# Performance work log

Hardware: AMD Instinct MI355X
Metric: run time of the kernel (lower is better)

## Reference

```python
import jax, jax.numpy as jnp
import numpy as np

B, S, I = 64, 32, 64
N_ITEMS = 100000
E, H = 256, 128


def setup_inputs() -> dict:
    key = jax.random.key(0)
    k_len, k_ids, k_ut, k_emb, k_wih, k_whh, k_a1, k_a2, k_vt = jax.random.split(key, 9)
    n_sess = B * S
    # ragged session lengths in [2, I] -> trailing zero padding, all sessions valid
    lengths = jax.random.randint(k_len, (n_sess,), 2, I + 1)
    ids = jax.random.randint(k_ids, (n_sess, I), 1, N_ITEMS + 1)
    pad_mask = jnp.arange(I)[None, :] < lengths[:, None]
    item_id = (ids * pad_mask).reshape(B, S, I).astype(jnp.int32)
    eval_from = jnp.zeros((B,), dtype=jnp.int32)
    u_type = jax.random.randint(k_ut, (B,), 0, 5).astype(jnp.int32)
    sc = 0.05
    emb = jax.random.normal(k_emb, (N_ITEMS + 1, E), jnp.float32) * sc
    emb = emb.at[0].set(0.0)  # padding_idx=0
    W_ih = jax.random.normal(k_wih, (3 * H, E), jnp.float32) * sc
    W_hh = jax.random.normal(k_whh, (3 * H, H), jnp.float32) * sc
    b_ih = jnp.zeros((3 * H,), jnp.float32)
    b_hh = jnp.zeros((3 * H,), jnp.float32)
    W_a1 = jax.random.normal(k_a1, (H, H), jnp.float32) * sc
    W_a2 = jax.random.normal(k_a2, (H, H), jnp.float32) * sc
    W_vt = jax.random.normal(k_vt, (1, H), jnp.float32) * sc
    return {"item_id": item_id, "eval_from": eval_from, "u_type": u_type,
            "emb": emb, "W_ih": W_ih, "W_hh": W_hh, "b_ih": b_ih, "b_hh": b_hh,
            "W_a1": W_a1, "W_a2": W_a2, "W_vt": W_vt}


def _gru(x, lengths, W_ih, W_hh, b_ih, b_hh):
    # x: [L, N, E]; packed-GRU semantics: state frozen past each length,
    # outputs zero at padded steps (matches pad_packed_sequence).
    L, N, _ = x.shape
    Hh = W_hh.shape[1]

    def step(h, inp):
        xt, t = inp
        gi = xt @ W_ih.T + b_ih           # [N, 3H]
        gh = h @ W_hh.T + b_hh
        i_r, i_z, i_n = jnp.split(gi, 3, axis=-1)
        h_r, h_z, h_n = jnp.split(gh, 3, axis=-1)
        r = jax.nn.sigmoid(i_r + h_r)
        z = jax.nn.sigmoid(i_z + h_z)
        n = jnp.tanh(i_n + r * h_n)
        h_new = (1.0 - z) * n + z * h
        valid = (t < lengths)[:, None]
        h_next = jnp.where(valid, h_new, h)
        out = jnp.where(valid, h_new, 0.0)
        return h_next, out

    h0 = jnp.zeros((N, Hh), x.dtype)
    hT, outs = jax.lax.scan(step, h0, (x, jnp.arange(L)))
    return outs, hT  # outs: [L, N, H], hT: [N, H]


def reference(item_id, eval_from, u_type, emb, W_ih, W_hh, b_ih, b_hh, W_a1, W_a2, W_vt):
    b, s, i = item_id.shape
    ids = jnp.clip(item_id, 0)
    allow = jnp.arange(s)[None, :] >= eval_from[:, None]        # [B, S]
    ids = ids * allow[:, :, None].astype(ids.dtype)
    sess = ids.reshape(b * s, i)                                # [N, I]
    lengths = (sess != 0).sum(1)                                # all >= 2 by construction
    n = sess.shape[0]
    target = sess[jnp.arange(n), lengths - 1]
    len_in = lengths - 1
    L = i - 1  # static L_in_max; extra padded steps are masked out
    mask = (jnp.arange(L)[None, :] < len_in[:, None])           # [N, L]
    inp = sess[:, :L] * mask.astype(sess.dtype)
    x = emb[inp]                                                # [N, L, E] (dropout=identity, eval)
    outs, ht = _gru(x.transpose(1, 0, 2), len_in, W_ih, W_hh, b_ih, b_hh)
    gru = outs.transpose(1, 0, 2)                               # [N, L, H]
    q1 = jnp.einsum('nlh,kh->nlk', gru, W_a1)
    q2 = (ht @ W_a2.T)[:, None, :]
    alpha = jnp.einsum('nlh,oh->nlo', jax.nn.sigmoid(q1 + q2), W_vt)[..., 0] * mask
    c_loc = jnp.einsum('nl,nlh->nh', alpha, gru)
    reps = jnp.concatenate([c_loc, ht], axis=1)                 # [N, 2H] (ct dropout=identity)
    u = jnp.repeat(u_type, s)
    return reps, target, u
```

## Files before the change

kernel.cpp:

```cpp
#include <hip/hip_runtime.h>
#include <hip/hip_bf16.h>

#define NSESS 2048
#define NI 64
#define LL 63
#define EE 256
#define HH 128
#define GG 384

typedef __attribute__((ext_vector_type(8))) short short8;
typedef __attribute__((ext_vector_type(4))) float f32x4;

static __device__ __forceinline__ unsigned short f2b(float f) {
  union { float f; unsigned u; } v; v.f = f;
  unsigned r = (v.u + 0x7FFFu + ((v.u >> 16) & 1u)) >> 16;
  return (unsigned short)r;
}
static __device__ __forceinline__ float b2f(unsigned short s) {
  union { unsigned u; float f; } v; v.u = ((unsigned)s) << 16;
  return v.f;
}
static __device__ __forceinline__ float sigmoidf_(float x) {
  return 1.f / (1.f + __expf(-x));
}
static __device__ __forceinline__ float tanh2_(float y) {
  float e = __expf(2.f * y);
  return 1.f - 2.f / (1.f + e);
}
static __device__ __forceinline__ void barrier_lds_only() {
  asm volatile("s_waitcnt lgkmcnt(0)" ::: "memory");
  __builtin_amdgcn_sched_barrier(0);
  __builtin_amdgcn_s_barrier();
  __builtin_amdgcn_sched_barrier(0);
}
static __device__ __forceinline__ void gload_lds16(const void* g, void* l) {
  __builtin_amdgcn_global_load_lds(
      (const __attribute__((address_space(1))) unsigned int*)g,
      (__attribute__((address_space(3))) unsigned int*)l, 16, 0, 0);
}

__global__ __launch_bounds__(64) void prep_kernel(const int* __restrict__ item_id,
                                                  const int* __restrict__ eval_from,
                                                  const int* __restrict__ u_type,
                                                  int* __restrict__ len_in,
                                                  int* __restrict__ inp,
                                                  float* __restrict__ out) {
  int n = blockIdx.x;
  int lane = threadIdx.x;
  int b = n >> 5, s = n & 31;
  int allow = (s >= eval_from[b]) ? 1 : 0;
  int id = item_id[n * NI + lane];
  if (id < 0) id = 0;
  id *= allow;
  unsigned long long m = __ballot(id != 0);
  int length = __popcll(m);
  int li = length - 1;
  int tv = __shfl(id, (length > 0) ? (length - 1) : 0, 64);
  int target = (length > 0) ? tv : 0;
  if (lane < LL) inp[n * LL + lane] = (lane < li) ? id : 0;
  if (lane == 0) {
    len_in[n] = li;
    out[NSESS * 256 + n] = (float)target;
    out[NSESS * 256 + NSESS + n] = (float)u_type[b];
  }
}

__global__ __launch_bounds__(256) void cvt_weights(const float* __restrict__ W_ih,
                                                   const float* __restrict__ W_hh,
                                                   const float* __restrict__ W_a1,
                                                   unsigned short* __restrict__ Wb,
                                                   unsigned short* __restrict__ Whs,
                                                   unsigned short* __restrict__ Wa1b) {
  int i = blockIdx.x * 256 + threadIdx.x;
  Wb[i] = f2b(W_ih[i]);
  if (i < GG * HH) Whs[i] = f2b(W_hh[i]);
  if (i < HH * HH) Wa1b[i] = f2b(W_a1[i]);
}

__global__ __launch_bounds__(512, 2) void gemm_in(const float* __restrict__ emb,
                                                  const unsigned short* __restrict__ Wb,
                                                  const float* __restrict__ b_ih,
                                                  const int* __restrict__ inp,
                                                  unsigned short* __restrict__ gi) {
  constexpr int XP = 264;
  __shared__ unsigned short Ash[2][16 * XP];

  const int t = threadIdx.x;
  const int lane = t & 63, w = t >> 6;
  const int ccol = lane & 15, kg = lane >> 4;
  const int g0 = w * 48;

  short8 bfr[3][8];
#pragma unroll
  for (int nt = 0; nt < 3; ++nt) {
    const unsigned short* wrow = Wb + (long)(g0 + nt * 16 + ccol) * EE + kg * 8;
#pragma unroll
    for (int c = 0; c < 8; ++c) bfr[nt][c] = *(const short8*)(wrow + c * 32);
  }
  float bias[3];
#pragma unroll
  for (int nt = 0; nt < 3; ++nt) bias[nt] = b_ih[g0 + nt * 16 + ccol];

  const int tile0 = blockIdx.x * 8;
  const int srow = t >> 5;
  const int scol = (t & 31) * 8;

  {
    long rid = inp[tile0 * 16 + srow];
    const float* x = emb + rid * EE + scol;
    float4 a0 = *(const float4*)x, a1 = *(const float4*)(x + 4);
    short8 v;
    v[0]=(short)f2b(a0.x); v[1]=(short)f2b(a0.y); v[2]=(short)f2b(a0.z); v[3]=(short)f2b(a0.w);
    v[4]=(short)f2b(a1.x); v[5]=(short)f2b(a1.y); v[6]=(short)f2b(a1.z); v[7]=(short)f2b(a1.w);
    *(short8*)(&Ash[0][srow * XP + scol]) = v;
  }
  __syncthreads();

  for (int i = 0; i < 8; ++i) {
    const int cur = i & 1;
    const int m0 = (tile0 + i) * 16;

    float4 a0, a1;
    if (i + 1 < 8) {
      long rid = inp[(tile0 + i + 1) * 16 + srow];
      const float* x = emb + rid * EE + scol;
      a0 = *(const float4*)x; a1 = *(const float4*)(x + 4);
    }

    f32x4 acc[3];
#pragma unroll
    for (int nt = 0; nt < 3; ++nt)
      acc[nt] = (f32x4){bias[nt], bias[nt], bias[nt], bias[nt]};
#pragma unroll
    for (int c = 0; c < 8; ++c) {
      short8 af = *(const short8*)(&Ash[cur][ccol * XP + c * 32 + kg * 8]);
#pragma unroll
      for (int nt = 0; nt < 3; ++nt)
        acc[nt] = __builtin_amdgcn_mfma_f32_16x16x32_bf16(af, bfr[nt][c], acc[nt], 0, 0, 0);
    }

    long base[4];
#pragma unroll
    for (int j = 0; j < 4; ++j) {
      int m = m0 + kg * 4 + j;
      int n = m / 63;
      int l = m - 63 * n;
      base[j] = ((long)l * NSESS + n) * GG;
    }
#pragma unroll
    for (int nt = 0; nt < 3; ++nt) {
      int g = g0 + nt * 16 + ccol;
#pragma unroll
      for (int j = 0; j < 4; ++j)
        gi[base[j] + g] = f2b(acc[nt][j]);
    }

    if (i + 1 < 8) {
      short8 v;
      v[0]=(short)f2b(a0.x); v[1]=(short)f2b(a0.y); v[2]=(short)f2b(a0.z); v[3]=(short)f2b(a0.w);
      v[4]=(short)f2b(a1.x); v[5]=(short)f2b(a1.y); v[6]=(short)f2b(a1.z); v[7]=(short)f2b(a1.w);
      *(short8*)(&Ash[cur ^ 1][srow * XP + scol]) = v;
    }
    barrier_lds_only();
  }
}

__global__ __launch_bounds__(512) void gru_mfma(const unsigned short* __restrict__ Whs,
                                                const float* __restrict__ b_hh,
                                                const unsigned short* __restrict__ gi,
                                                const int* __restrict__ len_in,
                                                unsigned short* __restrict__ outs,
                                                float* __restrict__ ht,
                                                float* __restrict__ out) {
  __shared__ unsigned short Gbuf[2 * 12288];
  __shared__ unsigned short ring[4 * 1024];

  const int t = threadIdx.x;
  const int w = t >> 6, lane = t & 63;
  const int ccol = lane & 15, kg = lane >> 4;
  const bool act = kg < 2;
  const int sbase = kg * 4;
  const int n0 = blockIdx.x * 8;
  const int jh = w * 16 + ccol;
  const int rr = ccol & 7;

  short8 bfr[3][4];
#pragma unroll
  for (int cls = 0; cls < 3; ++cls) {
    const unsigned short* wrow = Whs + (long)(cls * HH + jh) * HH;
#pragma unroll
    for (int c = 0; c < 4; ++c)
      bfr[cls][c] = *(const short8*)(wrow + c * 32 + kg * 8);
  }
  float bh[3];
#pragma unroll
  for (int cls = 0; cls < 3; ++cls) bh[cls] = b_hh[cls * HH + jh];

  int li[4];
#pragma unroll
  for (int r = 0; r < 4; ++r) li[r] = act ? len_in[n0 + sbase + r] : 0;
  float hold[4] = {0.f, 0.f, 0.f, 0.f};

  for (int idx = t; idx < 4096; idx += 512) ring[idx] = 0;

  const int dl4 = t >> 7, dsess = (t >> 4) & 7, dcol = (t & 15) * 8;
  const int dlen = len_in[n0 + dsess];

  auto do_stage = [&](int W2) {
    const int b = W2 & 1;
#pragma unroll
    for (int s = 0; s < 3; ++s) {
      int u = s * 512 + t;
      int ls = u / 384;
      int off = (u - ls * 384) * 8;
      int lg = 4 * W2 + ls; if (lg > 62) lg = 62;
      const unsigned short* src = gi + ((long)lg * NSESS + n0) * GG + off;
      gload_lds16(src, (char*)Gbuf + b * 24576 + u * 16);
    }
  };

  do_stage(0);
  do_stage(1);
  asm volatile("s_waitcnt vmcnt(3)" ::: "memory");
  __builtin_amdgcn_sched_barrier(0);
  barrier_lds_only();

  for (int W = 0; W < 16; ++W) {
    const unsigned short* gb_base = Gbuf + (W & 1) * 12288;
#pragma unroll
    for (int l2 = 0; l2 < 4; ++l2) {
      const int l = 4 * W + l2;
      if (l < LL) {
        const unsigned short* rb = ring + ((l + 3) & 3) * 1024 + rr * HH;
        short8 af[4];
#pragma unroll
        for (int c = 0; c < 4; ++c)
          af[c] = *(const short8*)(rb + ((c * 32 + kg * 8) ^ (rr << 3)));

        const unsigned short* gb = gb_base + l2 * 3072;
        float gvv[3][4];
        if (act) {
#pragma unroll
          for (int cls = 0; cls < 3; ++cls)
#pragma unroll
            for (int r = 0; r < 4; ++r)
              gvv[cls][r] = b2f(gb[(sbase + r) * GG + cls * HH + jh]);
        }

        f32x4 acc[3];
#pragma unroll
        for (int cls = 0; cls < 3; ++cls) {
          acc[cls] = (f32x4){bh[cls], bh[cls], bh[cls], bh[cls]};
#pragma unroll
          for (int c = 0; c < 4; ++c)
            acc[cls] = __builtin_amdgcn_mfma_f32_16x16x32_bf16(af[c], bfr[cls][c], acc[cls], 0, 0, 0);
        }

        if (act) {
          unsigned short* wrb = ring + (l & 3) * 1024;
#pragma unroll
          for (int r = 0; r < 4; ++r) {
            float rg = sigmoidf_(gvv[0][r] + acc[0][r]);
            float zg = sigmoidf_(gvv[1][r] + acc[1][r]);
            float ng = tanh2_(gvv[2][r] + rg * acc[2][r]);
            float hnew = ng + zg * (hold[r] - ng);
            hold[r] = (l < li[r]) ? hnew : hold[r];
            int sess = sbase + r;
            wrb[sess * HH + (jh ^ (sess << 3))] = f2b(hold[r]);
          }
        }
        barrier_lds_only();
      }
    }

    {
      const int dl = 4 * W + dl4;
      if (dl < LL) {
        short8 hv = *(const short8*)(ring + dl4 * 1024 + dsess * HH + (dcol ^ (dsess << 3)));
        if (dl >= dlen) hv = (short8){0, 0, 0, 0, 0, 0, 0, 0};
        *(short8*)(outs + ((long)(n0 + dsess) * LL + dl) * HH + dcol) = hv;
      }
    }
    if (W + 2 < 16) do_stage(W + 2);
    if (W < 14) {
      asm volatile("s_waitcnt vmcnt(4)" ::: "memory");
      __builtin_amdgcn_sched_barrier(0);
      barrier_lds_only();
    } else if (W == 14) {
      asm volatile("s_waitcnt vmcnt(1)" ::: "memory");
      __builtin_amdgcn_sched_barrier(0);
      barrier_lds_only();
    }
  }

  if (act) {
#pragma unroll
    for (int r = 0; r < 4; ++r) {
      int n = n0 + sbase + r;
      ht[(long)n * HH + jh] = hold[r];
      out[(long)n * 256 + HH + jh] = hold[r];
    }
  }
}

__global__ __launch_bounds__(256) void attn(const unsigned short* __restrict__ outs,
                                            const float* __restrict__ ht,
                                            const unsigned short* __restrict__ Wa1b,
                                            const float* __restrict__ W_a2,
                                            const float* __restrict__ W_vt,
                                            const int* __restrict__ len_in,
                                            float* __restrict__ out) {
  constexpr int OP = HH + 8;
  __shared__ unsigned short o_l[64 * OP];
  __shared__ float q2s[HH];
  __shared__ float wvt[HH];
  __shared__ float hts[HH];
  __shared__ float aw[4][64];
  __shared__ float alphas[64];

  const int n = blockIdx.x;
  const int t = threadIdx.x;
  const int lane = t & 63, wv = t >> 6;
  const int ccol = lane & 15, kg = lane >> 4;
  const int li = len_in[n];

  const unsigned* src = (const unsigned*)(outs + (long)n * LL * HH);
  for (int idx = t; idx < LL * 64; idx += 256) {
    int r = idx >> 6, c2 = idx & 63;
    ((unsigned*)(o_l + r * OP))[c2] = src[r * 64 + c2];
  }
  if (t < 64) ((unsigned*)(o_l + 63 * OP))[t] = 0;
  if (t < HH) { hts[t] = ht[(long)n * HH + t]; wvt[t] = W_vt[t]; }

  short8 bfr[2][4];
#pragma unroll
  for (int nt = 0; nt < 2; ++nt) {
    int G = wv * 32 + nt * 16 + ccol;
#pragma unroll
    for (int c = 0; c < 4; ++c)
      bfr[nt][c] = *(const short8*)(Wa1b + (long)G * HH + c * 32 + kg * 8);
  }
  __syncthreads();

  if (t < HH) {
    float a = 0.f;
    const float* w2 = W_a2 + t * HH;
    for (int k = 0; k < HH; ++k) a += hts[k] * w2[k];
    q2s[t] = a;
  }
  __syncthreads();

  f32x4 acc[4][2];
#pragma unroll
  for (int mt = 0; mt < 4; ++mt)
#pragma unroll
    for (int nt = 0; nt < 2; ++nt) acc[mt][nt] = (f32x4){0.f, 0.f, 0.f, 0.f};
#pragma unroll
  for (int mt = 0; mt < 4; ++mt) {
#pragma unroll
    for (int c = 0; c < 4; ++c) {
      short8 af = *(const short8*)(o_l + (mt * 16 + ccol) * OP + c * 32 + kg * 8);
#pragma unroll
      for (int nt = 0; nt < 2; ++nt)
        acc[mt][nt] = __builtin_amdgcn_mfma_f32_16x16x32_bf16(af, bfr[nt][c], acc[mt][nt], 0, 0, 0);
    }
  }

  float q2v[2], wvv[2];
#pragma unroll
  for (int nt = 0; nt < 2; ++nt) {
    int cg = wv * 32 + nt * 16 + ccol;
    q2v[nt] = q2s[cg]; wvv[nt] = wvt[cg];
  }
#pragma unroll
  for (int mt = 0; mt < 4; ++mt) {
    float part[4] = {0.f, 0.f, 0.f, 0.f};
#pragma unroll
    for (int nt = 0; nt < 2; ++nt)
#pragma unroll
      for (int j = 0; j < 4; ++j)
        part[j] += sigmoidf_(acc[mt][nt][j] + q2v[nt]) * wvv[nt];
#pragma unroll
    for (int j = 0; j < 4; ++j) {
#pragma unroll
      for (int off = 1; off < 16; off <<= 1)
        part[j] += __shfl_xor(part[j], off, 64);
    }
    if (ccol == 0) {
#pragma unroll
      for (int j = 0; j < 4; ++j) aw[wv][mt * 16 + kg * 4 + j] = part[j];
    }
  }
  __syncthreads();

  if (t < 64) {
    float s = aw[0][t] + aw[1][t] + aw[2][t] + aw[3][t];
    alphas[t] = (t < li) ? s : 0.f;
  }
  __syncthreads();

  if (t < HH) {
    float c = 0.f;
    for (int l = 0; l < LL; ++l) c = fmaf(alphas[l], b2f(o_l[l * OP + t]), c);
    out[(long)n * 256 + t] = c;
  }
}

extern "C" void kernel_launch(void* const* d_in, const int* in_sizes, int n_in,
                              void* d_out, int out_size, void* d_ws, size_t ws_size,
                              hipStream_t stream) {
  (void)in_sizes; (void)n_in; (void)out_size; (void)ws_size;
  const int* item_id   = (const int*)d_in[0];
  const int* eval_from = (const int*)d_in[1];
  const int* u_type    = (const int*)d_in[2];
  const float* emb     = (const float*)d_in[3];
  const float* W_ih    = (const float*)d_in[4];
  const float* W_hh    = (const float*)d_in[5];
  const float* b_ih    = (const float*)d_in[6];
  const float* b_hh    = (const float*)d_in[7];
  const float* W_a1    = (const float*)d_in[8];
  const float* W_a2    = (const float*)d_in[9];
  const float* W_vt    = (const float*)d_in[10];

  float* out = (float*)d_out;
  char* ws = (char*)d_ws;
  int* len_in           = (int*)(ws + 0);
  int* inp              = (int*)(ws + 8192);
  unsigned short* Wb    = (unsigned short*)(ws + 524288);
  unsigned short* Whs   = (unsigned short*)(ws + 720896);
  float* ht             = (float*)(ws + 819200);
  unsigned short* gi    = (unsigned short*)(ws + 1867776);
  unsigned short* outs  = (unsigned short*)(ws + 100958208);
  unsigned short* Wa1b  = (unsigned short*)(ws + 133988352);

  prep_kernel<<<NSESS, 64, 0, stream>>>(item_id, eval_from, u_type, len_in, inp, out);
  cvt_weights<<<384, 256, 0, stream>>>(W_ih, W_hh, W_a1, Wb, Whs, Wa1b);
  gemm_in<<<1008, 512, 0, stream>>>(emb, Wb, b_ih, inp, gi);
  gru_mfma<<<NSESS / 8, 512, 0, stream>>>(Whs, b_hh, gi, len_in, outs, ht, out);
  attn<<<NSESS, 512, 0, stream>>>(outs, ht, Wa1b, W_a2, W_vt, len_in, out);
}
```

Measured before the change: 155.6 us.

## Process 16 sessions per GRU block and prefetch gate inputs into registers

Each GRU block now handles 16 sessions instead of 8, so all four k-groups of the MFMA tile do useful work and the grid is halved. The staged global-to-LDS prefetch of gi is replaced by per-thread register double-buffering two timesteps ahead, and the hidden-state ring grows to 8 slots so output writeback reads the previous window's slots. This removes the idle lanes and the vmcnt/barrier staging, but leaves only 128 blocks on the GPU, which is fewer than the number of CUs, and it relies on scattered 2-byte global loads that must hide latency within two steps.

```diff
diff --git a/kernel.cpp b/kernel.cpp
--- a/kernel.cpp
+++ b/kernel.cpp
@@ -32,11 +32,6 @@
   __builtin_amdgcn_sched_barrier(0);
   __builtin_amdgcn_s_barrier();
   __builtin_amdgcn_sched_barrier(0);
-}
-static __device__ __forceinline__ void gload_lds16(const void* g, void* l) {
-  __builtin_amdgcn_global_load_lds(
-      (const __attribute__((address_space(1))) unsigned int*)g,
-      (__attribute__((address_space(3))) unsigned int*)l, 16, 0, 0);
 }
 
 __global__ __launch_bounds__(64) void prep_kernel(const int* __restrict__ item_id,
@@ -172,17 +167,15 @@
                                                 unsigned short* __restrict__ outs,
                                                 float* __restrict__ ht,
                                                 float* __restrict__ out) {
-  __shared__ unsigned short Gbuf[2 * 12288];
-  __shared__ unsigned short ring[4 * 1024];
+  __shared__ unsigned short ring[8 * 2048];
+  __shared__ int lens_s[16];
 
   const int t = threadIdx.x;
   const int w = t >> 6, lane = t & 63;
   const int ccol = lane & 15, kg = lane >> 4;
-  const bool act = kg < 2;
   const int sbase = kg * 4;
-  const int n0 = blockIdx.x * 8;
+  const int n0 = blockIdx.x * 16;
   const int jh = w * 16 + ccol;
-  const int rr = ccol & 7;
 
   short8 bfr[3][4];
 #pragma unroll
@@ -198,54 +191,52 @@
 
   int li[4];
 #pragma unroll
-  for (int r = 0; r < 4; ++r) li[r] = act ? len_in[n0 + sbase + r] : 0;
+  for (int r = 0; r < 4; ++r) li[r] = len_in[n0 + sbase + r];
   float hold[4] = {0.f, 0.f, 0.f, 0.f};
 
-  for (int idx = t; idx < 4096; idx += 512) ring[idx] = 0;
-
-  const int dl4 = t >> 7, dsess = (t >> 4) & 7, dcol = (t & 15) * 8;
-  const int dlen = len_in[n0 + dsess];
-
-  auto do_stage = [&](int W2) {
-    const int b = W2 & 1;
-#pragma unroll
-    for (int s = 0; s < 3; ++s) {
-      int u = s * 512 + t;
-      int ls = u / 384;
-      int off = (u - ls * 384) * 8;
-      int lg = 4 * W2 + ls; if (lg > 62) lg = 62;
-      const unsigned short* src = gi + ((long)lg * NSESS + n0) * GG + off;
-      gload_lds16(src, (char*)Gbuf + b * 24576 + u * 16);
-    }
-  };
-
-  do_stage(0);
-  do_stage(1);
-  asm volatile("s_waitcnt vmcnt(3)" ::: "memory");
-  __builtin_amdgcn_sched_barrier(0);
+  for (int idx = t; idx < 8 * 2048; idx += 512) ring[idx] = 0;
+  if (t < 16) lens_s[t] = len_in[n0 + t];
+
+  const unsigned short* gbase = gi + (long)(n0 + sbase) * GG + jh;
+  const long lstride = (long)NSESS * GG;
+#define GADDR(l, cls, r) (gbase + (long)(l) * lstride + (r) * GG + (cls) * HH)
+
+  unsigned short gA[12], gB[12];
+#pragma unroll
+  for (int k = 0; k < 12; ++k) gA[k] = *GADDR(0, k >> 2, k & 3);
+#pragma unroll
+  for (int k = 0; k < 12; ++k) gB[k] = *GADDR(1, k >> 2, k & 3);
+
   barrier_lds_only();
 
   for (int W = 0; W < 16; ++W) {
-    const unsigned short* gb_base = Gbuf + (W & 1) * 12288;
 #pragma unroll
     for (int l2 = 0; l2 < 4; ++l2) {
       const int l = 4 * W + l2;
       if (l < LL) {
-        const unsigned short* rb = ring + ((l + 3) & 3) * 1024 + rr * HH;
+        float gvv[12];
+        if ((l2 & 1) == 0) {
+#pragma unroll
+          for (int k = 0; k < 12; ++k) gvv[k] = b2f(gA[k]);
+        } else {
+#pragma unroll
+          for (int k = 0; k < 12; ++k) gvv[k] = b2f(gB[k]);
+        }
+        if (l + 2 < LL) {
+          if ((l2 & 1) == 0) {
+#pragma unroll
+            for (int k = 0; k < 12; ++k) gA[k] = *GADDR(l + 2, k >> 2, k & 3);
+          } else {
+#pragma unroll
+            for (int k = 0; k < 12; ++k) gB[k] = *GADDR(l + 2, k >> 2, k & 3);
+          }
+        }
+
+        const unsigned short* rb = ring + ((l + 7) & 7) * 2048 + ccol * HH;
         short8 af[4];
 #pragma unroll
         for (int c = 0; c < 4; ++c)
-          af[c] = *(const short8*)(rb + ((c * 32 + kg * 8) ^ (rr << 3)));
-
-        const unsigned short* gb = gb_base + l2 * 3072;
-        float gvv[3][4];
-        if (act) {
-#pragma unroll
-          for (int cls = 0; cls < 3; ++cls)
-#pragma unroll
-            for (int r = 0; r < 4; ++r)
-              gvv[cls][r] = b2f(gb[(sbase + r) * GG + cls * HH + jh]);
-        }
+          af[c] = *(const short8*)(rb + ((c * 32 + kg * 8) ^ ((ccol & 7) << 3)));
 
         f32x4 acc[3];
 #pragma unroll
@@ -256,50 +247,42 @@
             acc[cls] = __builtin_amdgcn_mfma_f32_16x16x32_bf16(af[c], bfr[cls][c], acc[cls], 0, 0, 0);
         }
 
-        if (act) {
-          unsigned short* wrb = ring + (l & 3) * 1024;
-#pragma unroll
-          for (int r = 0; r < 4; ++r) {
-            float rg = sigmoidf_(gvv[0][r] + acc[0][r]);
-            float zg = sigmoidf_(gvv[1][r] + acc[1][r]);
-            float ng = tanh2_(gvv[2][r] + rg * acc[2][r]);
-            float hnew = ng + zg * (hold[r] - ng);
-            hold[r] = (l < li[r]) ? hnew : hold[r];
-            int sess = sbase + r;
-            wrb[sess * HH + (jh ^ (sess << 3))] = f2b(hold[r]);
-          }
+        unsigned short* wrb = ring + (l & 7) * 2048;
+#pragma unroll
+        for (int r = 0; r < 4; ++r) {
+          float rg = sigmoidf_(gvv[0 * 4 + r] + acc[0][r]);
+          float zg = sigmoidf_(gvv[1 * 4 + r] + acc[1][r]);
+          float ng = tanh2_(gvv[2 * 4 + r] + rg * acc[2][r]);
+          float hnew = ng + zg * (hold[r] - ng);
+          hold[r] = (l < li[r]) ? hnew : hold[r];
+          int sess = sbase + r;
+          wrb[sess * HH + (jh ^ ((sess & 7) << 3))] = f2b(hold[r]);
         }
         barrier_lds_only();
       }
     }
 
-    {
-      const int dl = 4 * W + dl4;
+#pragma unroll
+    for (int half = 0; half < 2; ++half) {
+      int idx = half * 512 + t;
+      int dl2 = idx >> 8, sess = (idx >> 4) & 15, col8 = (idx & 15) * 8;
+      int dl = 4 * W + dl2;
       if (dl < LL) {
-        short8 hv = *(const short8*)(ring + dl4 * 1024 + dsess * HH + (dcol ^ (dsess << 3)));
-        if (dl >= dlen) hv = (short8){0, 0, 0, 0, 0, 0, 0, 0};
-        *(short8*)(outs + ((long)(n0 + dsess) * LL + dl) * HH + dcol) = hv;
+        int slot = (W & 1) * 4 + dl2;
+        short8 hv = *(const short8*)(ring + slot * 2048 + sess * HH +
+                                     (col8 ^ ((sess & 7) << 3)));
+        if (dl >= lens_s[sess]) hv = (short8){0, 0, 0, 0, 0, 0, 0, 0};
+        *(short8*)(outs + ((long)(n0 + sess) * LL + dl) * HH + col8) = hv;
       }
     }
-    if (W + 2 < 16) do_stage(W + 2);
-    if (W < 14) {
-      asm volatile("s_waitcnt vmcnt(4)" ::: "memory");
-      __builtin_amdgcn_sched_barrier(0);
-      barrier_lds_only();
-    } else if (W == 14) {
-      asm volatile("s_waitcnt vmcnt(1)" ::: "memory");
-      __builtin_amdgcn_sched_barrier(0);
-      barrier_lds_only();
-    }
-  }
-
-  if (act) {
-#pragma unroll
-    for (int r = 0; r < 4; ++r) {
-      int n = n0 + sbase + r;
-      ht[(long)n * HH + jh] = hold[r];
-      out[(long)n * 256 + HH + jh] = hold[r];
-    }
+  }
+#undef GADDR
+
+#pragma unroll
+  for (int r = 0; r < 4; ++r) {
+    int n = n0 + sbase + r;
+    ht[(long)n * HH + jh] = hold[r];
+    out[(long)n * 256 + HH + jh] = hold[r];
   }
 }
 
@@ -436,6 +419,6 @@
   prep_kernel<<<NSESS, 64, 0, stream>>>(item_id, eval_from, u_type, len_in, inp, out);
   cvt_weights<<<384, 256, 0, stream>>>(W_ih, W_hh, W_a1, Wb, Whs, Wa1b);
   gemm_in<<<1008, 512, 0, stream>>>(emb, Wb, b_ih, inp, gi);
-  gru_mfma<<<NSESS / 8, 512, 0, stream>>>(Whs, b_hh, gi, len_in, outs, ht, out);
+  gru_mfma<<<NSESS / 16, 512, 0, stream>>>(Whs, b_hh, gi, len_in, outs, ht, out);
   attn<<<NSESS, 512, 0, stream>>>(outs, ht, Wa1b, W_a2, W_vt, len_in, out);
 }
```

Measured after the change: 163.0 us. 1.05x slower.
